# Kernel tuning notes

Hardware: AMD Instinct MI355X
Metric: run time of the kernel (lower is better)

Reference implementation:

```python
import jax, jax.numpy as jnp
import numpy as np

WEIGHT = 1.0  # init kwarg
B, N, M, D = 32, 128, 128, 256


def _hungarian(cost):
    """O(n^3) Hungarian (Jonker-Volgenant potentials form) on host numpy.
    cost: [n, m] with n <= m. Returns col index assigned to each row
    (row_ind is implicitly arange(n), matching scipy.linear_sum_assignment).
    """
    cost = np.asarray(cost, dtype=np.float64)
    n, m = cost.shape
    u = np.zeros(n + 1)
    v = np.zeros(m + 1)
    p = np.zeros(m + 1, dtype=np.int64)   # p[j] = row (1-based) matched to col j
    way = np.zeros(m + 1, dtype=np.int64)
    for i in range(1, n + 1):
        p[0] = i
        j0 = 0
        minv = np.full(m + 1, np.inf)
        used = np.zeros(m + 1, dtype=bool)
        while True:
            used[j0] = True
            i0 = p[j0]
            free = ~used[1:]
            cur = cost[i0 - 1, :] - u[i0] - v[1:]
            upd = free & (cur < minv[1:])
            minv[1:][upd] = cur[upd]
            way[1:][upd] = j0
            masked = np.where(free, minv[1:], np.inf)
            j1 = int(np.argmin(masked)) + 1
            delta = masked[j1 - 1]
            u[p[used]] += delta
            v[used] -= delta
            minv[1:][free] -= delta
            j0 = j1
            if p[j0] == 0:
                break
        while j0:
            j1 = way[j0]
            p[j0] = p[j1]
            j0 = j1
    col_of_row = np.zeros(n, dtype=np.int64)
    for j in range(1, m + 1):
        if p[j] > 0:
            col_of_row[p[j] - 1] = j - 1
    return col_of_row


def _pairwise_mse(p, g):
    """cost[b,i,j] = mean_d (p[b,i,d]-g[b,j,d])^2, fused without [B,N,M,D] tensor."""
    d = p.shape[-1]
    p2 = jnp.sum(p * p, axis=-1)                    # [B,N]
    g2 = jnp.sum(g * g, axis=-1)                    # [B,M]
    pg = jnp.einsum('bnd,bmd->bnm', p, g)           # [B,N,M]
    return (p2[:, :, None] + g2[:, None, :] - 2.0 * pg) / d


def setup_inputs() -> dict:
    key = jax.random.key(0)
    k1, k2 = jax.random.split(key)
    batch_prediction = jax.random.normal(k1, (B, N, D), dtype=jnp.float32)
    batch_groundtruth = jax.random.normal(k2, (B, M, D), dtype=jnp.float32)
    return {"batch_prediction": batch_prediction,
            "batch_groundtruth": batch_groundtruth}


def reference(batch_prediction, batch_groundtruth):
    b, n = batch_prediction.shape[0], batch_prediction.shape[1]
    cost = _pairwise_mse(batch_prediction, batch_groundtruth)   # [B,N,M]
    cost_np = np.asarray(jax.device_get(cost))
    # Hungarian assignment on host (matches scipy.linear_sum_assignment; CPU-bound)
    cols = jnp.asarray(np.stack([_hungarian(cost_np[bi]) for bi in range(b)]))  # [B,N]
    matched = cost[jnp.arange(b)[:, None], jnp.arange(n)[None, :], cols]        # [B,N]
    loss = matched.mean(axis=1).sum() / b * WEIGHT
    return jnp.reshape(loss, (1,))
```

## Files before the change

### kernel.cpp

```cpp
#include <hip/hip_runtime.h>
#include <float.h>

#define Bc 32
#define Nn 128
#define Dd 256

template <int CTRL>
__device__ __forceinline__ float dpp_addsrc(float x) {
    return __int_as_float(__builtin_amdgcn_update_dpp(0, __float_as_int(x), CTRL,
                                                      0xf, 0xf, false));
}
__device__ __forceinline__ float wave_sum_lane63(float x) {
    x += dpp_addsrc<0x121>(x);
    x += dpp_addsrc<0x122>(x);
    x += dpp_addsrc<0x124>(x);
    x += dpp_addsrc<0x128>(x);
    x += dpp_addsrc<0x142>(x);
    x += dpp_addsrc<0x143>(x);
    return x;
}

template <int CTRL>
__device__ __forceinline__ unsigned dpp_movu(unsigned x) {
    return (unsigned)__builtin_amdgcn_update_dpp((int)0xFFFFFFFFu, (int)x, CTRL,
                                                 0xf, 0xf, false);
}
__device__ __forceinline__ unsigned wave_umin_lane63(unsigned x) {
    x = min(x, dpp_movu<0x121>(x));
    x = min(x, dpp_movu<0x122>(x));
    x = min(x, dpp_movu<0x124>(x));
    x = min(x, dpp_movu<0x128>(x));
    x = min(x, dpp_movu<0x142>(x));
    x = min(x, dpp_movu<0x143>(x));
    return x;
}

template <int CTRL>
__device__ __forceinline__ float dpp_movf(float x) {
    return __int_as_float(__builtin_amdgcn_update_dpp(0x7f7fffff, __float_as_int(x),
                                                      CTRL, 0xf, 0xf, false));
}
template <int CTRL>
__device__ __forceinline__ void dpp2min_step(float& m1, float& m2) {
    float o1 = dpp_movf<CTRL>(m1);
    float o2 = dpp_movf<CTRL>(m2);
    float n1 = fminf(m1, o1);
    m2 = fminf(fmaxf(m1, o1), fminf(m2, o2));
    m1 = n1;
}

__device__ __forceinline__ float readlane_f(float v, int lane) {
    return __int_as_float(__builtin_amdgcn_readlane(__float_as_int(v), lane));
}

__global__ __launch_bounds__(64) void cost_kernel(const float* __restrict__ P,
                                                  const float* __restrict__ G,
                                                  float* __restrict__ C,
                                                  float* __restrict__ out) {
    const int b = blockIdx.y;
    const int i = blockIdx.x;
    const int t = threadIdx.x;

    if (b == 0 && i == 0 && t == 0) *out = 0.0f;

    const float4 pv = ((const float4*)(P + ((size_t)b * Nn + i) * Dd))[t];
    const float4* g4 = (const float4*)(G + (size_t)b * Nn * Dd);
    float* crow = C + ((size_t)b * Nn + i) * Nn;

    for (int j = 0; j < Nn; j += 2) {
        float4 gv0 = g4[(size_t)j * 64 + t];
        float4 gv1 = g4[(size_t)(j + 1) * 64 + t];
        float dx0 = pv.x - gv0.x, dy0 = pv.y - gv0.y, dz0 = pv.z - gv0.z, dw0 = pv.w - gv0.w;
        float dx1 = pv.x - gv1.x, dy1 = pv.y - gv1.y, dz1 = pv.z - gv1.z, dw1 = pv.w - gv1.w;
        float s0 = dx0 * dx0 + dy0 * dy0 + dz0 * dz0 + dw0 * dw0;
        float s1 = dx1 * dx1 + dy1 * dy1 + dz1 * dz1 + dw1 * dw1;
        s0 = wave_sum_lane63(s0);
        s1 = wave_sum_lane63(s1);
        if (t == 63) {
            crow[j]     = s0 * (1.0f / (float)Dd);
            crow[j + 1] = s1 * (1.0f / (float)Dd);
        }
    }
}

__global__ __launch_bounds__(64) void hungarian_kernel(const float* __restrict__ Call,
                                                       float* __restrict__ out) {
    const int b = blockIdx.x;
    const int t = threadIdx.x;

    __shared__ float Csh[Nn * Nn];
    __shared__ int claim[Nn];

    {
        const float4* src = (const float4*)(Call + (size_t)b * Nn * Nn);
        float4* dst = (float4*)Csh;
#pragma unroll
        for (int k = 0; k < (Nn * Nn / 4) / 64; ++k)
            dst[k * 64 + t] = src[k * 64 + t];
    }
    claim[t] = 0x7fffffff;
    claim[t + 64] = 0x7fffffff;
    __syncthreads();

    float bestA = FLT_MAX, bestB = FLT_MAX;
    int argA = 0, argB = 0;
    for (int i = 0; i < Nn; ++i) {
        float c0 = Csh[i * Nn + t];
        float c1 = Csh[i * Nn + t + 64];
        if (c0 < bestA) { bestA = c0; argA = i; }
        if (c1 < bestB) { bestB = c1; argB = i; }
    }
    float vA = bestA, vB = bestB;
    atomicMin(&claim[argA], t);
    atomicMin(&claim[argB], t + 64);
    __syncthreads();

    float uA = 0.0f, uB = 0.0f;
    float wA = 0.0f, wB = 0.0f;
    int pA = 0, pB = 0;
    if (claim[argA] == t)      pA = argA + 1;
    if (claim[argB] == t + 64) pB = argB + 1;

    unsigned long long fmA = __ballot(claim[t] == 0x7fffffff);
    unsigned long long fmB = __ballot(claim[t + 64] == 0x7fffffff);

    {
        int rcA = claim[t];
        int rcB = claim[t + 64];
        float c0 = Csh[t];
        float c1 = Csh[t + 64];
        for (int r = 0; r < Nn; ++r) {
            int s_c = __builtin_amdgcn_readlane((r & 64) ? rcB : rcA, r & 63);
            int pr = (r + 1) & (Nn - 1);
            float n0 = Csh[pr * Nn + t];
            float n1 = Csh[pr * Nn + t + 64];
            if (s_c != 0x7fffffff) {
                bool ex0 = (t == s_c);
                bool ex1 = (t + 64 == s_c);
                float cur0 = ex0 ? FLT_MAX : (c0 - vA);
                float cur1 = ex1 ? FLT_MAX : (c1 - vB);
                float m = fminf(cur0, cur1);
                m = fminf(m, dpp_movf<0x121>(m));
                m = fminf(m, dpp_movf<0x122>(m));
                m = fminf(m, dpp_movf<0x124>(m));
                m = fminf(m, dpp_movf<0x128>(m));
                m = fminf(m, dpp_movf<0x142>(m));
                m = fminf(m, dpp_movf<0x143>(m));
                float mu = readlane_f(m, 63);
                if (ex0) { vA -= mu; wA = mu; }
                if (ex1) { vB -= mu; wB = mu; }
                if (t == (r & 63)) {
                    if (r < 64) uA = mu; else uB = mu;
                }
            }
            c0 = n0; c1 = n1;
        }
    }

    for (int pass = 0; pass < 2; ++pass) {
        if (!(fmA | fmB)) break;
        unsigned long long remA = fmA, remB = fmB;
        int guard = 0;
        while ((remA | remB) != 0ull && guard++ < 256) {
            int l, i, slotR;
            if (remA) { l = __ffsll(remA) - 1; remA &= remA - 1; i = l + 1;  slotR = 0;
                        if (!((fmA >> l) & 1)) continue; }
            else      { l = __ffsll(remB) - 1; remB &= remB - 1; i = l + 65; slotR = 1;
                        if (!((fmB >> l) & 1)) continue; }

            const float* crow = &Csh[(i - 1) * Nn];
            float cur0 = crow[t] - vA;
            float cur1 = crow[t + 64] - vB;
            float m1 = fminf(cur0, cur1);
            float m2 = fmaxf(cur0, cur1);
            dpp2min_step<0x121>(m1, m2);
            dpp2min_step<0x122>(m1, m2);
            dpp2min_step<0x124>(m1, m2);
            dpp2min_step<0x128>(m1, m2);
            dpp2min_step<0x142>(m1, m2);
            dpp2min_step<0x143>(m1, m2);
            float s_m1 = readlane_f(m1, 63);
            float s_m2 = readlane_f(m2, 63);

            unsigned long long b0 = __ballot(cur0 == s_m1);
            unsigned long long b1 = __ballot(cur1 == s_m1);
            int j1 = b0 ? __ffsll(b0) : (__ffsll(b1) + 64);
            int lane1 = (j1 - 1) & 63, slot1 = (j1 - 1) >> 6;

            if (t == l) { if (slotR == 0) uA = s_m2; else uB = s_m2; }

            int k0 = __builtin_amdgcn_readlane(slot1 ? pB : pA, lane1);
            bool strict = (s_m1 < s_m2);
            if (!strict && k0 != 0) continue;

            if (t == lane1) {
                if (slot1 == 0) { vA += s_m1 - s_m2; pA = i; wA = s_m2; }
                else            { vB += s_m1 - s_m2; pB = i; wB = s_m2; }
            }
            if (slotR == 0) fmA &= ~(1ull << l); else fmB &= ~(1ull << l);
            if (k0 != 0) {
                int kl = (k0 - 1) & 63;
                if (k0 <= 64) { fmA |= 1ull << kl; remA |= 1ull << kl; }
                else          { fmB |= 1ull << kl; remB |= 1ull << kl; }
            }
        }
    }

    for (int slotR = 0; slotR < 2; ++slotR) {
        unsigned long long mask = slotR ? fmB : fmA;
        while (mask) {
            int l = __ffsll(mask) - 1;
            mask &= mask - 1;
            int i = l + 1 + slotR * 64;

            float minvA = FLT_MAX, minvB = FLT_MAX;
            int wayA = 0, wayB = 0;
            bool usedA = false, usedB = false;
            bool rUA = false, rUB = false;
            if (t == l) { if (slotR == 0) rUA = true; else rUB = true; }

            int s_j0 = 0;
            float s_u = readlane_f(slotR ? uB : uA, l);
            int s_j1;

            float c0 = Csh[(i - 1) * Nn + t];
            float c1 = Csh[(i - 1) * Nn + t + 64];

            for (;;) {
                if (!usedA) {
                    float cur = fmaxf(c0 - s_u - vA, 0.0f);
                    if (cur < minvA) { minvA = cur; wayA = s_j0; }
                }
                if (!usedB) {
                    float cur = fmaxf(c1 - s_u - vB, 0.0f);
                    if (cur < minvB) { minvB = cur; wayB = s_j0; }
                }

                unsigned kA = (__float_as_uint(usedA ? FLT_MAX : minvA) & 0xFFFFFF00u)
                              | (unsigned)t;
                unsigned kB = (__float_as_uint(usedB ? FLT_MAX : minvB) & 0xFFFFFF00u)
                              | (unsigned)(t + 64);
                unsigned k = wave_umin_lane63(min(kA, kB));
                unsigned s_key = (unsigned)__builtin_amdgcn_readlane((int)k, 63);
                float s_delta = __uint_as_float(s_key & 0xFFFFFF00u);
                s_j1 = (int)(s_key & 0xFFu) + 1;

                int lane1 = (s_j1 - 1) & 63;
                int slot1 = (s_j1 - 1) >> 6;
                int s_p = __builtin_amdgcn_readlane(slot1 ? pB : pA, lane1);
                float s_w = readlane_f(slot1 ? wB : wA, lane1);

                int nrow = (s_p > 0 ? s_p : 1) - 1;
                float nc0 = Csh[nrow * Nn + t];
                float nc1 = Csh[nrow * Nn + t + 64];

                if (usedA) { vA -= s_delta; wA += s_delta; }
                else       { minvA = fmaxf(minvA - s_delta, 0.0f); }
                if (usedB) { vB -= s_delta; wB += s_delta; }
                else       { minvB = fmaxf(minvB - s_delta, 0.0f); }
                if (rUA) uA += s_delta;
                if (rUB) uB += s_delta;

                if (s_p == 0) break;

                if (t == lane1) { if (slot1 == 0) usedA = true; else usedB = true; }
                {
                    int r = s_p - 1;
                    if (t == (r & 63)) { if ((r >> 6) == 0) rUA = true; else rUB = true; }
                }
                s_j0 = s_j1;
                s_u = s_w;
                c0 = nc0;
                c1 = nc1;
            }

            int s_j = s_j1;
            while (s_j) {
                int lane = (s_j - 1) & 63;
                int slot = (s_j - 1) >> 6;
                int s_jprev = __builtin_amdgcn_readlane(slot ? wayB : wayA, lane);
                int s_pnew;
                if (s_jprev == 0) {
                    s_pnew = i;
                } else {
                    int lp = (s_jprev - 1) & 63;
                    int sp = (s_jprev - 1) >> 6;
                    s_pnew = __builtin_amdgcn_readlane(sp ? pB : pA, lp);
                }
                int rl = (s_pnew - 1) & 63;
                int rs = (s_pnew - 1) >> 6;
                float s_unew = readlane_f(rs ? uB : uA, rl);
                if (t == lane) {
                    if (slot == 0) { pA = s_pnew; wA = s_unew; }
                    else           { pB = s_pnew; wB = s_unew; }
                }
                s_j = s_jprev;
            }
        }
    }

    float tot = Csh[(pA - 1) * Nn + t] + Csh[(pB - 1) * Nn + t + 64];
    tot = wave_sum_lane63(tot);

    if (t == 63) {
        atomicAdd(out, tot * (1.0f / ((float)Nn * (float)Bc)));
    }
}

extern "C" void kernel_launch(void* const* d_in, const int* in_sizes, int n_in,
                              void* d_out, int out_size, void* d_ws, size_t ws_size,
                              hipStream_t stream) {
    const float* P = (const float*)d_in[0];
    const float* G = (const float*)d_in[1];
    float* out = (float*)d_out;
    float* C = (float*)d_ws;

    dim3 gcost(Nn, Bc);
    cost_kernel<<<gcost, 64, 0, stream>>>(P, G, C, out);
    hungarian_kernel<<<Bc, 64, 0, stream>>>(C, out);
}
```

Before: 534.6 us.

## Interleave two Hungarian problems per wave as state machines to hide latency

Each block now handles two batch items. It loads both cost matrices into dynamic LDS (about 128KB) and advances their augmenting-path searches as interleaved state machines, one step per tick. The goal is to overlap the serial latency chains (DPP reductions, readlanes, LDS loads) of two independent problems in a single wave. In exchange the grid shrinks from 32 blocks to 16, so each wave does more serial work, and the loop runs until the slower of the two problems finishes.

```diff
diff --git a/kernel.cpp b/kernel.cpp
--- a/kernel.cpp
+++ b/kernel.cpp
@@ -83,57 +83,39 @@
     }
 }
 
-__global__ __launch_bounds__(64) void hungarian_kernel(const float* __restrict__ Call,
-                                                       float* __restrict__ out) {
-    const int b = blockIdx.x;
-    const int t = threadIdx.x;
-
-    __shared__ float Csh[Nn * Nn];
-    __shared__ int claim[Nn];
-
-    {
-        const float4* src = (const float4*)(Call + (size_t)b * Nn * Nn);
-        float4* dst = (float4*)Csh;
-#pragma unroll
-        for (int k = 0; k < (Nn * Nn / 4) / 64; ++k)
-            dst[k * 64 + t] = src[k * 64 + t];
-    }
-    claim[t] = 0x7fffffff;
-    claim[t + 64] = 0x7fffffff;
-    __syncthreads();
-
+__device__ __forceinline__ void phases12(const float* __restrict__ CS, int* clm, int t,
+        float& vA, float& vB, float& uA, float& uB, float& wA, float& wB,
+        int& pA, int& pB, unsigned long long& fmA, unsigned long long& fmB) {
     float bestA = FLT_MAX, bestB = FLT_MAX;
     int argA = 0, argB = 0;
     for (int i = 0; i < Nn; ++i) {
-        float c0 = Csh[i * Nn + t];
-        float c1 = Csh[i * Nn + t + 64];
+        float c0 = CS[i * Nn + t];
+        float c1 = CS[i * Nn + t + 64];
         if (c0 < bestA) { bestA = c0; argA = i; }
         if (c1 < bestB) { bestB = c1; argB = i; }
     }
-    float vA = bestA, vB = bestB;
-    atomicMin(&claim[argA], t);
-    atomicMin(&claim[argB], t + 64);
+    vA = bestA; vB = bestB;
+    atomicMin(&clm[argA], t);
+    atomicMin(&clm[argB], t + 64);
     __syncthreads();
 
-    float uA = 0.0f, uB = 0.0f;
-    float wA = 0.0f, wB = 0.0f;
-    int pA = 0, pB = 0;
-    if (claim[argA] == t)      pA = argA + 1;
-    if (claim[argB] == t + 64) pB = argB + 1;
-
-    unsigned long long fmA = __ballot(claim[t] == 0x7fffffff);
-    unsigned long long fmB = __ballot(claim[t + 64] == 0x7fffffff);
+    uA = 0.0f; uB = 0.0f; wA = 0.0f; wB = 0.0f;
+    pA = 0; pB = 0;
+    if (clm[argA] == t)      pA = argA + 1;
+    if (clm[argB] == t + 64) pB = argB + 1;
+    fmA = __ballot(clm[t] == 0x7fffffff);
+    fmB = __ballot(clm[t + 64] == 0x7fffffff);
 
     {
-        int rcA = claim[t];
-        int rcB = claim[t + 64];
-        float c0 = Csh[t];
-        float c1 = Csh[t + 64];
+        int rcA = clm[t];
+        int rcB = clm[t + 64];
+        float c0 = CS[t];
+        float c1 = CS[t + 64];
         for (int r = 0; r < Nn; ++r) {
             int s_c = __builtin_amdgcn_readlane((r & 64) ? rcB : rcA, r & 63);
             int pr = (r + 1) & (Nn - 1);
-            float n0 = Csh[pr * Nn + t];
-            float n1 = Csh[pr * Nn + t + 64];
+            float n0 = CS[pr * Nn + t];
+            float n1 = CS[pr * Nn + t + 64];
             if (s_c != 0x7fffffff) {
                 bool ex0 = (t == s_c);
                 bool ex1 = (t + 64 == s_c);
@@ -168,7 +150,7 @@
             else      { l = __ffsll(remB) - 1; remB &= remB - 1; i = l + 65; slotR = 1;
                         if (!((fmB >> l) & 1)) continue; }
 
-            const float* crow = &Csh[(i - 1) * Nn];
+            const float* crow = &CS[(i - 1) * Nn];
             float cur0 = crow[t] - vA;
             float cur1 = crow[t + 64] - vB;
             float m1 = fminf(cur0, cur1);
@@ -205,75 +187,52 @@
             }
         }
     }
-
-    for (int slotR = 0; slotR < 2; ++slotR) {
-        unsigned long long mask = slotR ? fmB : fmA;
-        while (mask) {
-            int l = __ffsll(mask) - 1;
-            mask &= mask - 1;
-            int i = l + 1 + slotR * 64;
-
-            float minvA = FLT_MAX, minvB = FLT_MAX;
-            int wayA = 0, wayB = 0;
-            bool usedA = false, usedB = false;
-            bool rUA = false, rUB = false;
-            if (t == l) { if (slotR == 0) rUA = true; else rUB = true; }
-
-            int s_j0 = 0;
-            float s_u = readlane_f(slotR ? uB : uA, l);
-            int s_j1;
-
-            float c0 = Csh[(i - 1) * Nn + t];
-            float c1 = Csh[(i - 1) * Nn + t + 64];
-
-            for (;;) {
-                if (!usedA) {
-                    float cur = fmaxf(c0 - s_u - vA, 0.0f);
-                    if (cur < minvA) { minvA = cur; wayA = s_j0; }
-                }
-                if (!usedB) {
-                    float cur = fmaxf(c1 - s_u - vB, 0.0f);
-                    if (cur < minvB) { minvB = cur; wayB = s_j0; }
-                }
-
-                unsigned kA = (__float_as_uint(usedA ? FLT_MAX : minvA) & 0xFFFFFF00u)
-                              | (unsigned)t;
-                unsigned kB = (__float_as_uint(usedB ? FLT_MAX : minvB) & 0xFFFFFF00u)
-                              | (unsigned)(t + 64);
-                unsigned k = wave_umin_lane63(min(kA, kB));
-                unsigned s_key = (unsigned)__builtin_amdgcn_readlane((int)k, 63);
-                float s_delta = __uint_as_float(s_key & 0xFFFFFF00u);
-                s_j1 = (int)(s_key & 0xFFu) + 1;
-
-                int lane1 = (s_j1 - 1) & 63;
-                int slot1 = (s_j1 - 1) >> 6;
-                int s_p = __builtin_amdgcn_readlane(slot1 ? pB : pA, lane1);
-                float s_w = readlane_f(slot1 ? wB : wA, lane1);
-
-                int nrow = (s_p > 0 ? s_p : 1) - 1;
-                float nc0 = Csh[nrow * Nn + t];
-                float nc1 = Csh[nrow * Nn + t + 64];
-
-                if (usedA) { vA -= s_delta; wA += s_delta; }
-                else       { minvA = fmaxf(minvA - s_delta, 0.0f); }
-                if (usedB) { vB -= s_delta; wB += s_delta; }
-                else       { minvB = fmaxf(minvB - s_delta, 0.0f); }
-                if (rUA) uA += s_delta;
-                if (rUB) uB += s_delta;
-
-                if (s_p == 0) break;
-
-                if (t == lane1) { if (slot1 == 0) usedA = true; else usedB = true; }
-                {
-                    int r = s_p - 1;
-                    if (t == (r & 63)) { if ((r >> 6) == 0) rUA = true; else rUB = true; }
-                }
-                s_j0 = s_j1;
-                s_u = s_w;
-                c0 = nc0;
-                c1 = nc1;
-            }
-
+}
+
+__device__ __forceinline__ void dijk_tick(const float* __restrict__ CS, int t,
+        int& st, unsigned long long& mA, unsigned long long& mB,
+        int& i_cur, float& s_u, int& s_j0,
+        float& vA, float& vB, float& uA, float& uB, float& wA, float& wB,
+        int& pA, int& pB,
+        float& minvA, float& minvB, int& wayA, int& wayB,
+        float& c0, float& c1,
+        bool& usedA, bool& usedB, bool& rUA, bool& rUB) {
+    if (st == 1) {
+        if (!usedA) {
+            float cur = fmaxf(c0 - s_u - vA, 0.0f);
+            if (cur < minvA) { minvA = cur; wayA = s_j0; }
+        }
+        if (!usedB) {
+            float cur = fmaxf(c1 - s_u - vB, 0.0f);
+            if (cur < minvB) { minvB = cur; wayB = s_j0; }
+        }
+
+        unsigned kA = (__float_as_uint(usedA ? FLT_MAX : minvA) & 0xFFFFFF00u)
+                      | (unsigned)t;
+        unsigned kB = (__float_as_uint(usedB ? FLT_MAX : minvB) & 0xFFFFFF00u)
+                      | (unsigned)(t + 64);
+        unsigned k = wave_umin_lane63(min(kA, kB));
+        unsigned s_key = (unsigned)__builtin_amdgcn_readlane((int)k, 63);
+        float s_delta = __uint_as_float(s_key & 0xFFFFFF00u);
+        int s_j1 = (int)(s_key & 0xFFu) + 1;
+
+        int lane1 = (s_j1 - 1) & 63;
+        int slot1 = (s_j1 - 1) >> 6;
+        int s_p = __builtin_amdgcn_readlane(slot1 ? pB : pA, lane1);
+        float s_w = readlane_f(slot1 ? wB : wA, lane1);
+
+        int nrow = (s_p > 0 ? s_p : 1) - 1;
+        float nc0 = CS[nrow * Nn + t];
+        float nc1 = CS[nrow * Nn + t + 64];
+
+        if (usedA) { vA -= s_delta; wA += s_delta; }
+        else       { minvA = fmaxf(minvA - s_delta, 0.0f); }
+        if (usedB) { vB -= s_delta; wB += s_delta; }
+        else       { minvB = fmaxf(minvB - s_delta, 0.0f); }
+        if (rUA) uA += s_delta;
+        if (rUB) uB += s_delta;
+
+        if (s_p == 0) {
             int s_j = s_j1;
             while (s_j) {
                 int lane = (s_j - 1) & 63;
@@ -281,7 +240,7 @@
                 int s_jprev = __builtin_amdgcn_readlane(slot ? wayB : wayA, lane);
                 int s_pnew;
                 if (s_jprev == 0) {
-                    s_pnew = i;
+                    s_pnew = i_cur;
                 } else {
                     int lp = (s_jprev - 1) & 63;
                     int sp = (s_jprev - 1) >> 6;
@@ -296,10 +255,93 @@
                 }
                 s_j = s_jprev;
             }
-        }
-    }
-
-    float tot = Csh[(pA - 1) * Nn + t] + Csh[(pB - 1) * Nn + t + 64];
+            st = 0;
+        } else {
+            if (t == lane1) { if (slot1 == 0) usedA = true; else usedB = true; }
+            {
+                int r = s_p - 1;
+                if (t == (r & 63)) { if ((r >> 6) == 0) rUA = true; else rUB = true; }
+            }
+            s_j0 = s_j1;
+            s_u = s_w;
+            c0 = nc0;
+            c1 = nc1;
+        }
+    }
+    if (st == 0) {
+        if ((mA | mB) == 0ull) { st = 2; return; }
+        int l, slotR;
+        if (mA) { l = __ffsll(mA) - 1; mA &= mA - 1; slotR = 0; }
+        else    { l = __ffsll(mB) - 1; mB &= mB - 1; slotR = 1; }
+        i_cur = l + 1 + slotR * 64;
+        minvA = FLT_MAX; minvB = FLT_MAX;
+        wayA = 0; wayB = 0;
+        usedA = false; usedB = false;
+        rUA = (slotR == 0) && (t == l);
+        rUB = (slotR == 1) && (t == l);
+        s_j0 = 0;
+        s_u = readlane_f(slotR ? uB : uA, l);
+        c0 = CS[(i_cur - 1) * Nn + t];
+        c1 = CS[(i_cur - 1) * Nn + t + 64];
+        st = 1;
+    }
+}
+
+__global__ __launch_bounds__(64) void hungarian_kernel(const float* __restrict__ Call,
+                                                       float* __restrict__ out) {
+    const int bid = blockIdx.x;
+    const int t = threadIdx.x;
+
+    extern __shared__ __align__(16) float smem[];
+    float* Csh0 = smem;
+    float* Csh1 = smem + Nn * Nn;
+    int* claim = (int*)(smem + 2 * Nn * Nn);
+
+    {
+        const float4* src0 = (const float4*)(Call + (size_t)(2 * bid) * Nn * Nn);
+        const float4* src1 = (const float4*)(Call + (size_t)(2 * bid + 1) * Nn * Nn);
+        float4* dst0 = (float4*)Csh0;
+        float4* dst1 = (float4*)Csh1;
+#pragma unroll
+        for (int k = 0; k < (Nn * Nn / 4) / 64; ++k) dst0[k * 64 + t] = src0[k * 64 + t];
+#pragma unroll
+        for (int k = 0; k < (Nn * Nn / 4) / 64; ++k) dst1[k * 64 + t] = src1[k * 64 + t];
+    }
+    claim[t] = 0x7fffffff;       claim[t + 64] = 0x7fffffff;
+    claim[t + 128] = 0x7fffffff; claim[t + 192] = 0x7fffffff;
+    __syncthreads();
+
+    float vA0, vB0, uA0, uB0, wA0, wB0;
+    float vA1, vB1, uA1, uB1, wA1, wB1;
+    int pA0, pB0, pA1, pB1;
+    unsigned long long fmA0, fmB0, fmA1, fmB1;
+
+    phases12(Csh0, claim,      t, vA0, vB0, uA0, uB0, wA0, wB0, pA0, pB0, fmA0, fmB0);
+    phases12(Csh1, claim + Nn, t, vA1, vB1, uA1, uB1, wA1, wB1, pA1, pB1, fmA1, fmB1);
+
+    int st0 = 0, st1 = 0;
+    int i0 = 1, i1 = 1;
+    float su0 = 0.0f, su1 = 0.0f;
+    int j00 = 0, j01 = 0;
+    float minvA0 = FLT_MAX, minvB0 = FLT_MAX, minvA1 = FLT_MAX, minvB1 = FLT_MAX;
+    int wayA0 = 0, wayB0 = 0, wayA1 = 0, wayB1 = 0;
+    float c00 = 0.0f, c10 = 0.0f, c01 = 0.0f, c11 = 0.0f;
+    bool usedA0 = false, usedB0 = false, usedA1 = false, usedB1 = false;
+    bool rUA0 = false, rUB0 = false, rUA1 = false, rUB1 = false;
+
+    while (st0 != 2 || st1 != 2) {
+        dijk_tick(Csh0, t, st0, fmA0, fmB0, i0, su0, j00,
+                  vA0, vB0, uA0, uB0, wA0, wB0, pA0, pB0,
+                  minvA0, minvB0, wayA0, wayB0, c00, c10,
+                  usedA0, usedB0, rUA0, rUB0);
+        dijk_tick(Csh1, t, st1, fmA1, fmB1, i1, su1, j01,
+                  vA1, vB1, uA1, uB1, wA1, wB1, pA1, pB1,
+                  minvA1, minvB1, wayA1, wayB1, c01, c11,
+                  usedA1, usedB1, rUA1, rUB1);
+    }
+
+    float tot = Csh0[(pA0 - 1) * Nn + t] + Csh0[(pB0 - 1) * Nn + t + 64]
+              + Csh1[(pA1 - 1) * Nn + t] + Csh1[(pB1 - 1) * Nn + t + 64];
     tot = wave_sum_lane63(tot);
 
     if (t == 63) {
@@ -315,7 +357,17 @@
     float* out = (float*)d_out;
     float* C = (float*)d_ws;
 
+    const int lds_bytes = 2 * Nn * Nn * (int)sizeof(float) + 2 * Nn * (int)sizeof(int);
+
+    static bool attr_set = false;
+    if (!attr_set) {
+        (void)hipFuncSetAttribute((const void*)hungarian_kernel,
+                                  hipFuncAttributeMaxDynamicSharedMemorySize,
+                                  lds_bytes);
+        attr_set = true;
+    }
+
     dim3 gcost(Nn, Bc);
     cost_kernel<<<gcost, 64, 0, stream>>>(P, G, C, out);
-    hungarian_kernel<<<Bc, 64, 0, stream>>>(C, out);
-}
+    hungarian_kernel<<<Bc / 2, 64, lds_bytes, stream>>>(C, out);
+}
```

Result: slower. 1.465 ms (+174.0%).
